# Optimization experiments

Measured on AMD Instinct MI355X. Metric: run time of the kernel, lower is better.

Reference implementation:

```python
import jax, jax.numpy as jnp
import numpy as np

N, E, DIN, DH = 50000, 1600000, 128, 128
P_DROP = 0.5


def setup_inputs() -> dict:
    key = jax.random.key(0)
    ks = jax.random.split(key, 9)
    scale = 0.05
    x = jax.random.normal(ks[0], (N, DIN), jnp.float32)
    edge_index = jax.random.randint(ks[1], (2, E), 0, N, dtype=jnp.int32)
    W0 = jax.random.normal(ks[2], (DH, DIN), jnp.float32) * scale
    b0 = jnp.zeros((DH,), jnp.float32)
    W1 = jax.random.normal(ks[3], (DH, DH), jnp.float32) * scale
    b1 = jnp.zeros((DH,), jnp.float32)
    W2 = jax.random.normal(ks[4], (DH, DH), jnp.float32) * scale
    b2 = jnp.zeros((DH,), jnp.float32)
    # deterministic inverted-dropout mask (train-mode Dropout(p=0.5))
    drop_mask = jax.random.bernoulli(ks[5], 1.0 - P_DROP, (N, DH)).astype(jnp.float32) / (1.0 - P_DROP)
    return {"x": x, "edge_index": edge_index, "drop_mask": drop_mask,
            "W0": W0, "b0": b0, "W1": W1, "b1": b1, "W2": W2, "b2": b2}


def _gcn_conv(h_in, W, b, src, dst, dinv):
    # PyG GCNConv: linear -> symmetric-normalized aggregation with self loops -> bias
    h = h_in @ W.T                                   # [N, out]
    norm = dinv[src] * dinv[dst]                      # [E]
    msg = h[src] * norm[:, None]                      # [E, out]
    out = jax.ops.segment_sum(msg, dst, num_segments=N)
    out = out + h * (dinv * dinv)[:, None]            # self-loop contribution
    return out + b


def reference(x, edge_index, drop_mask, W0, b0, W1, b1, W2, b2):
    src, dst = edge_index[0], edge_index[1]
    # degree of target nodes, +1 for the added self loop (shared by all layers)
    deg = jax.ops.segment_sum(jnp.ones((E,), x.dtype), dst, num_segments=N) + 1.0
    dinv = jax.lax.rsqrt(deg)

    h = _gcn_conv(x, W0, b0, src, dst, dinv)
    h = jax.nn.relu(h * drop_mask)                    # Dropout(0.5) then ReLU
    x_ = _gcn_conv(h, W1, b1, src, dst, dinv)
    x2 = _gcn_conv(h, W2, b2, src, dst, dinv)         # conv2 also consumes h (as in source)
    return (x_, x2)
```

## Files before the change

kernel.cpp:

```cpp
#include <hip/hip_runtime.h>


#define D 128
#define BK_SHIFT 7
#define BK_NODES 128
#define NBMAX 512
#define CAP 7936
#define TILE_A 2048

typedef __attribute__((ext_vector_type(8))) short bf16x8;
typedef __attribute__((ext_vector_type(4))) float f32x4;

static __device__ __forceinline__ unsigned f2bf(float f) {
  union { float f; unsigned u; } v; v.f = f;
  unsigned r = v.u + 0x7FFF + ((v.u >> 16) & 1);
  return r >> 16;
}
static __device__ __forceinline__ float bflo(unsigned u) {
  return __uint_as_float(u << 16);
}
static __device__ __forceinline__ float bfhi(unsigned u) {
  return __uint_as_float(u & 0xFFFF0000u);
}


__global__ __launch_bounds__(256) void k_bucketA(const int* __restrict__ src,
                                                 const int* __restrict__ dst,
                                                 int* __restrict__ bcnt,
                                                 int* __restrict__ packed,
                                                 const float* __restrict__ W0,
                                                 const float* __restrict__ W1,
                                                 const float* __restrict__ W2,
                                                 unsigned short* __restrict__ Wb,
                                                 int E, int nb) {
  __shared__ int hist[NBMAX];
  __shared__ int base[NBMAX];
  __shared__ unsigned pv[TILE_A];
  int t = threadIdx.x;
  int e0 = blockIdx.x * TILE_A;

  if (blockIdx.x < 192) {
    int i = blockIdx.x * 256 + t;
    const float* W = (i < 16384) ? W0 : (i < 32768 ? W1 : W2);
    Wb[i] = (unsigned short)f2bf(W[i & 16383]);
  }

  for (int b = t; b < nb; b += 256) hist[b] = 0;
  __syncthreads();

  for (int i = t; i < TILE_A; i += 256) {
    int e = e0 + i;
    if (e < E) {
      int d = dst[e];
      int s = src[e];
      unsigned bkt = (unsigned)d >> BK_SHIFT;
      pv[i] = (unsigned)(s & 0xFFFF) | ((unsigned)(d & (BK_NODES - 1)) << 16) |
              (bkt << 23);
      atomicAdd(&hist[bkt], 1);
    }
  }
  __syncthreads();

  for (int b = t; b < nb; b += 256) {
    int h = hist[b];
    if (h) base[b] = atomicAdd(&bcnt[b], h);
  }
  __syncthreads();

  for (int i = t; i < TILE_A; i += 256) {
    int e = e0 + i;
    if (e < E) {
      unsigned v = pv[i];
      unsigned bkt = v >> 23;
      int pos = atomicAdd(&base[bkt], 1);
      if (pos < CAP) packed[(size_t)bkt * CAP + pos] = (int)(v & 0x7FFFFF);
    }
  }
}

__global__ __launch_bounds__(512) void k_bucketB2(const int* __restrict__ packed,
                                                  const int* __restrict__ bcnt,
                                                  int* __restrict__ gcur,
                                                  int* __restrict__ srcSorted,
                                                  int* __restrict__ rowBeg,
                                                  int* __restrict__ rowEnd,
                                                  float* __restrict__ dinv,
                                                  int n) {
  __shared__ int histC[BK_NODES];
  __shared__ int cur[BK_NODES];
  __shared__ int buf[CAP];
  __shared__ int obase;
  int t = threadIdx.x;
  int bkt = blockIdx.x;
  int n0 = bkt << BK_SHIFT;
  int beg = bkt * CAP;
  int cnt = bcnt[bkt];
  if (cnt > CAP) cnt = CAP;

  if (t < BK_NODES) histC[t] = 0;
  __syncthreads();

  for (int i = t; i < cnt; i += 512)
    atomicAdd(&histC[packed[beg + i] >> 16], 1);
  __syncthreads();

  if (t == 0) {
    int run = 0;
#pragma unroll
    for (int j = 0; j < BK_NODES; ++j) { cur[j] = run; run += histC[j]; }
    obase = atomicAdd(gcur, run);
  }
  __syncthreads();

  if (t < BK_NODES && n0 + t < n) {
    int rb = obase + cur[t];
    rowBeg[n0 + t] = rb;
    rowEnd[n0 + t] = rb + histC[t];
    dinv[n0 + t]   = rsqrtf((float)histC[t] + 1.0f);
  }
  __syncthreads();

  for (int i = t; i < cnt; i += 512) {
    int p = packed[beg + i];
    int pos = atomicAdd(&cur[p >> 16], 1);
    buf[pos] = p & 0xFFFF;
  }
  __syncthreads();
  for (int i = t; i < cnt; i += 512)
    srcSorted[obase + i] = buf[i] << 8;
}


template <int EPI>
__global__ __launch_bounds__(256) void k_aggb(const unsigned* __restrict__ T,
                                              const int* __restrict__ srcSorted,
                                              const int* __restrict__ rowBeg,
                                              const int* __restrict__ rowEnd,
                                              const float* __restrict__ dinv,
                                              const float* __restrict__ bias,
                                              const float* __restrict__ mask,
                                              unsigned* __restrict__ outB,
                                              int n) {
  int wave = (blockIdx.x * 256 + threadIdx.x) >> 6;
  int lane = threadIdx.x & 63;
  if (wave >= n) return;
  const char* Tb = (const char*)T;
  int lo = lane << 2;
  int beg = rowBeg[wave], end = rowEnd[wave];
  float a0x = 0.f, a0y = 0.f, a1x = 0.f, a1y = 0.f;
  float a2x = 0.f, a2y = 0.f, a3x = 0.f, a3y = 0.f;
  int j = beg;
  for (; j + 15 < end; j += 16) {
    unsigned u[16];
#pragma unroll
    for (int q = 0; q < 16; ++q)
      u[q] = *(const unsigned*)(Tb + srcSorted[j + q] + lo);
#pragma unroll
    for (int q = 0; q < 16; q += 4) {
      a0x += bflo(u[q + 0]);  a0y += bfhi(u[q + 0]);
      a1x += bflo(u[q + 1]);  a1y += bfhi(u[q + 1]);
      a2x += bflo(u[q + 2]);  a2y += bfhi(u[q + 2]);
      a3x += bflo(u[q + 3]);  a3y += bfhi(u[q + 3]);
    }
  }
  for (; j + 7 < end; j += 8) {
    unsigned u[8];
#pragma unroll
    for (int q = 0; q < 8; ++q)
      u[q] = *(const unsigned*)(Tb + srcSorted[j + q] + lo);
#pragma unroll
    for (int q = 0; q < 8; q += 4) {
      a0x += bflo(u[q + 0]);  a0y += bfhi(u[q + 0]);
      a1x += bflo(u[q + 1]);  a1y += bfhi(u[q + 1]);
      a2x += bflo(u[q + 2]);  a2y += bfhi(u[q + 2]);
      a3x += bflo(u[q + 3]);  a3y += bfhi(u[q + 3]);
    }
  }
  for (; j < end; ++j) {
    unsigned u = *(const unsigned*)(Tb + srcSorted[j] + lo);
    a0x += bflo(u);
    a0y += bfhi(u);
  }
  unsigned us = T[(size_t)wave * 64 + lane];
  float dn = dinv[wave];
  float ox = ((a0x + a1x) + (a2x + a3x) + bflo(us)) * dn;
  float oy = ((a0y + a1y) + (a2y + a3y) + bfhi(us)) * dn;
  if (EPI == 1) {
    float2 bv = ((const float2*)bias)[lane];
    float2 mv = ((const float2*)mask)[(size_t)wave * 64 + lane];
    float hx = fmaxf((ox + bv.x) * mv.x, 0.f);
    float hy = fmaxf((oy + bv.y) * mv.y, 0.f);
    outB[(size_t)wave * 64 + lane] = f2bf(hx * dn) | (f2bf(hy * dn) << 16);
  } else {
    outB[(size_t)wave * 64 + lane] = f2bf(ox) | (f2bf(oy) << 16);
  }
}


template <bool BF16IN, bool BF16OUT>
__global__ __launch_bounds__(256) void k_gemm_mfma(const void* __restrict__ Xv,
                                                   const unsigned short* __restrict__ Wb,
                                                   const float* __restrict__ bias,
                                                   const float* __restrict__ prescale,
                                                   float* __restrict__ Cf,
                                                   unsigned short* __restrict__ Cb,
                                                   int nrows) {
  int wid  = threadIdx.x >> 6;
  int lane = threadIdx.x & 63;
  int r0   = blockIdx.x * 64 + wid * 16;
  int arow = r0 + (lane & 15);
  int kb   = (lane >> 4) * 8;
  bool rowok = arow < nrows;

  bf16x8 a[4];
  if (BF16IN) {
    const unsigned short* X = (const unsigned short*)Xv;
#pragma unroll
    for (int ks = 0; ks < 4; ++ks) {
      bf16x8 t;
      if (rowok) t = *reinterpret_cast<const bf16x8*>(X + (size_t)arow * D + ks * 32 + kb);
      else { for (int q = 0; q < 8; ++q) t[q] = 0; }
      a[ks] = t;
    }
  } else {
    const float* X = (const float*)Xv;
#pragma unroll
    for (int ks = 0; ks < 4; ++ks) {
      bf16x8 t;
      if (rowok) {
        const float* p = X + (size_t)arow * D + ks * 32 + kb;
        float4 f0 = *(const float4*)(p);
        float4 f1 = *(const float4*)(p + 4);
        t[0] = (short)f2bf(f0.x); t[1] = (short)f2bf(f0.y);
        t[2] = (short)f2bf(f0.z); t[3] = (short)f2bf(f0.w);
        t[4] = (short)f2bf(f1.x); t[5] = (short)f2bf(f1.y);
        t[6] = (short)f2bf(f1.z); t[7] = (short)f2bf(f1.w);
      } else {
        for (int q = 0; q < 8; ++q) t[q] = 0;
      }
      a[ks] = t;
    }
  }

  int rbase = r0 + (lane >> 4) * 4;
  float sc[4];
  if (BF16OUT) {
#pragma unroll
    for (int reg = 0; reg < 4; ++reg) {
      int rr = rbase + reg;
      sc[reg] = (prescale && rr < nrows) ? prescale[rr] : 1.0f;
    }
  }

#pragma unroll
  for (int ct = 0; ct < 8; ++ct) {
    int col = ct * 16 + (lane & 15);
    f32x4 acc = {0.f, 0.f, 0.f, 0.f};
#pragma unroll
    for (int ks = 0; ks < 4; ++ks) {
      bf16x8 b = *reinterpret_cast<const bf16x8*>(Wb + (size_t)col * D + ks * 32 + kb);
      acc = __builtin_amdgcn_mfma_f32_16x16x32_bf16(a[ks], b, acc, 0, 0, 0);
    }
    if (BF16OUT) {
#pragma unroll
      for (int reg = 0; reg < 4; ++reg) {
        int rr = rbase + reg;
        if (rr < nrows)
          Cb[(size_t)rr * D + col] = (unsigned short)f2bf(acc[reg] * sc[reg]);
      }
    } else {
      float bc = bias ? bias[col] : 0.f;
#pragma unroll
      for (int reg = 0; reg < 4; ++reg) {
        int rr = rbase + reg;
        if (rr < nrows) Cf[(size_t)rr * D + col] = acc[reg] + bc;
      }
    }
  }
}

__global__ __launch_bounds__(256) void k_gemm_mfma2(const unsigned short* __restrict__ X,
                                                    const unsigned short* __restrict__ W1b,
                                                    const unsigned short* __restrict__ W2b,
                                                    const float* __restrict__ b1,
                                                    const float* __restrict__ b2,
                                                    float* __restrict__ C1,
                                                    float* __restrict__ C2,
                                                    int nrows) {
  int wid  = threadIdx.x >> 6;
  int lane = threadIdx.x & 63;
  int r0   = blockIdx.x * 64 + wid * 16;
  int arow = r0 + (lane & 15);
  int kb   = (lane >> 4) * 8;
  bool rowok = arow < nrows;

  bf16x8 a[4];
#pragma unroll
  for (int ks = 0; ks < 4; ++ks) {
    bf16x8 t;
    if (rowok) t = *reinterpret_cast<const bf16x8*>(X + (size_t)arow * D + ks * 32 + kb);
    else { for (int q = 0; q < 8; ++q) t[q] = 0; }
    a[ks] = t;
  }

  int rbase = r0 + (lane >> 4) * 4;

#pragma unroll
  for (int wm = 0; wm < 2; ++wm) {
    const unsigned short* Wb = (wm == 0) ? W1b : W2b;
    const float* bias        = (wm == 0) ? b1 : b2;
    float* Cf                = (wm == 0) ? C1 : C2;
#pragma unroll
    for (int ct = 0; ct < 8; ++ct) {
      int col = ct * 16 + (lane & 15);
      f32x4 acc = {0.f, 0.f, 0.f, 0.f};
#pragma unroll
      for (int ks = 0; ks < 4; ++ks) {
        bf16x8 b = *reinterpret_cast<const bf16x8*>(Wb + (size_t)col * D + ks * 32 + kb);
        acc = __builtin_amdgcn_mfma_f32_16x16x32_bf16(a[ks], b, acc, 0, 0, 0);
      }
      float bc = bias[col];
#pragma unroll
      for (int reg = 0; reg < 4; ++reg) {
        int rr = rbase + reg;
        if (rr < nrows) Cf[(size_t)rr * D + col] = acc[reg] + bc;
      }
    }
  }
}


__global__ __launch_bounds__(256) void k_deg_f(const int* __restrict__ dst,
                                               float* __restrict__ deg, int E) {
  int i = blockIdx.x * 256 + threadIdx.x;
  if (i < E) atomicAdd(&deg[dst[i]], 1.0f);
}

__global__ __launch_bounds__(256) void k_dinv_f(float* __restrict__ deg, int n) {
  int i = blockIdx.x * 256 + threadIdx.x;
  if (i < n) deg[i] = rsqrtf(deg[i] + 1.0f);
}

__global__ __launch_bounds__(256) void k_selfmul(const float* __restrict__ X,
                                                 const float* __restrict__ dinv,
                                                 float* __restrict__ out, int n) {
  int i = blockIdx.x * 256 + threadIdx.x;
  if (i >= n * 32) return;
  int r = i >> 5, c4 = (i & 31) << 2;
  float di = dinv[r];
  float s = di * di;
  float4 h = *(const float4*)(X + (size_t)r * D + c4);
  h.x *= s; h.y *= s; h.z *= s; h.w *= s;
  *(float4*)(out + (size_t)r * D + c4) = h;
}

__global__ __launch_bounds__(256) void k_relumask(float* __restrict__ h,
                                                  const float* __restrict__ mask, int n) {
  int i = blockIdx.x * 256 + threadIdx.x;
  if (i >= n * 32) return;
  float4 v = *(const float4*)(h + (size_t)i * 4);
  float4 m = *(const float4*)(mask + (size_t)i * 4);
  v.x = fmaxf(v.x * m.x, 0.f);
  v.y = fmaxf(v.y * m.y, 0.f);
  v.z = fmaxf(v.z * m.z, 0.f);
  v.w = fmaxf(v.w * m.w, 0.f);
  *(float4*)(h + (size_t)i * 4) = v;
}

__global__ __launch_bounds__(256) void k_aggatomic(const float* __restrict__ X,
                                                   const int* __restrict__ src,
                                                   const int* __restrict__ dst,
                                                   const float* __restrict__ dinv,
                                                   float* __restrict__ out, int E) {
  int gid = blockIdx.x * 256 + threadIdx.x;
  int wave = gid >> 6;
  int lane = threadIdx.x & 63;
  int nw = (gridDim.x * 256) >> 6;
  for (int e = wave; e < E; e += nw) {
    int s = src[e], d = dst[e];
    float nrm = dinv[s] * dinv[d];
    float2 v = ((const float2*)(X + (size_t)s * D))[lane];
    float* op = out + (size_t)d * D + lane * 2;
    atomicAdd(op, v.x * nrm);
    atomicAdd(op + 1, v.y * nrm);
  }
}

__global__ __launch_bounds__(256) void k_addbias(float* __restrict__ C,
                                                 const float* __restrict__ bias, int n) {
  int i = blockIdx.x * 256 + threadIdx.x;
  if (i >= n * 32) return;
  int c4 = (i & 31) << 2;
  float4 v = *(const float4*)(C + (size_t)i * 4);
  float4 b = *(const float4*)(bias + c4);
  v.x += b.x; v.y += b.y; v.z += b.z; v.w += b.w;
  *(float4*)(C + (size_t)i * 4) = v;
}

template <bool BF16OUT>
__global__ __launch_bounds__(256) void k_gemm128(const float* __restrict__ X,
                                                 const float* __restrict__ W,
                                                 const float* __restrict__ bias,
                                                 const float* __restrict__ prescale,
                                                 float* __restrict__ Cf,
                                                 unsigned short* __restrict__ Cb,
                                                 int nrows) {
  __shared__ float Xs[64][132];
  __shared__ float Ws[32][128];

  int tid = threadIdx.x;
  int row0 = blockIdx.x * 64;

  for (int t = tid; t < 2048; t += 256) {
    int r = t >> 5;
    int c4 = (t & 31) << 2;
    int gr = row0 + r;
    float4 v = make_float4(0.f, 0.f, 0.f, 0.f);
    if (gr < nrows) v = *(const float4*)(X + (size_t)gr * D + c4);
    Xs[r][c4 + 0] = v.x; Xs[r][c4 + 1] = v.y;
    Xs[r][c4 + 2] = v.z; Xs[r][c4 + 3] = v.w;
  }

  float acc[4][8];
#pragma unroll
  for (int i = 0; i < 4; ++i)
#pragma unroll
    for (int j = 0; j < 8; ++j) acc[i][j] = 0.f;

  int ty = tid >> 4, tx = tid & 15;
  int r0 = ty << 2, c0 = tx << 3;

  for (int k0 = 0; k0 < 128; k0 += 32) {
    int j = tid >> 1;
    int kkb = (tid & 1) << 4;
    const float4* wp = (const float4*)(W + j * D + k0 + kkb);
    float4 wa = wp[0], wb = wp[1], wc = wp[2], wd = wp[3];

    __syncthreads();
    Ws[kkb +  0][j] = wa.x; Ws[kkb +  1][j] = wa.y; Ws[kkb +  2][j] = wa.z; Ws[kkb +  3][j] = wa.w;
    Ws[kkb +  4][j] = wb.x; Ws[kkb +  5][j] = wb.y; Ws[kkb +  6][j] = wb.z; Ws[kkb +  7][j] = wb.w;
    Ws[kkb +  8][j] = wc.x; Ws[kkb +  9][j] = wc.y; Ws[kkb + 10][j] = wc.z; Ws[kkb + 11][j] = wc.w;
    Ws[kkb + 12][j] = wd.x; Ws[kkb + 13][j] = wd.y; Ws[kkb + 14][j] = wd.z; Ws[kkb + 15][j] = wd.w;
    __syncthreads();

#pragma unroll
    for (int kk = 0; kk < 32; ++kk) {
      float xi[4];
      xi[0] = Xs[r0 + 0][k0 + kk];
      xi[1] = Xs[r0 + 1][k0 + kk];
      xi[2] = Xs[r0 + 2][k0 + kk];
      xi[3] = Xs[r0 + 3][k0 + kk];
      float4 wv0 = *(const float4*)(&Ws[kk][c0]);
      float4 wv1 = *(const float4*)(&Ws[kk][c0 + 4]);
      float wf[8] = {wv0.x, wv0.y, wv0.z, wv0.w, wv1.x, wv1.y, wv1.z, wv1.w};
#pragma unroll
      for (int i = 0; i < 4; ++i)
#pragma unroll
        for (int jj = 0; jj < 8; ++jj) acc[i][jj] += xi[i] * wf[jj];
    }
  }

  float4 bv0 = make_float4(0.f, 0.f, 0.f, 0.f);
  float4 bv1 = make_float4(0.f, 0.f, 0.f, 0.f);
  if (bias) {
    bv0 = *(const float4*)(bias + c0);
    bv1 = *(const float4*)(bias + c0 + 4);
  }

#pragma unroll
  for (int i = 0; i < 4; ++i) {
    int gr = row0 + r0 + i;
    if (gr < nrows) {
      float o[8];
      o[0] = acc[i][0] + bv0.x; o[1] = acc[i][1] + bv0.y;
      o[2] = acc[i][2] + bv0.z; o[3] = acc[i][3] + bv0.w;
      o[4] = acc[i][4] + bv1.x; o[5] = acc[i][5] + bv1.y;
      o[6] = acc[i][6] + bv1.z; o[7] = acc[i][7] + bv1.w;
      if (BF16OUT) {
        float dn = prescale ? prescale[gr] : 1.0f;
        uint4 pk;
        pk.x = f2bf(o[0] * dn) | (f2bf(o[1] * dn) << 16);
        pk.y = f2bf(o[2] * dn) | (f2bf(o[3] * dn) << 16);
        pk.z = f2bf(o[4] * dn) | (f2bf(o[5] * dn) << 16);
        pk.w = f2bf(o[6] * dn) | (f2bf(o[7] * dn) << 16);
        *(uint4*)(Cb + (size_t)gr * D + c0) = pk;
      } else {
        *(float4*)(Cf + (size_t)gr * D + c0)     = make_float4(o[0], o[1], o[2], o[3]);
        *(float4*)(Cf + (size_t)gr * D + c0 + 4) = make_float4(o[4], o[5], o[6], o[7]);
      }
    }
  }
}


extern "C" void kernel_launch(void* const* d_in, const int* in_sizes, int n_in,
                              void* d_out, int out_size, void* d_ws, size_t ws_size,
                              hipStream_t stream) {
  const float* x    = (const float*)d_in[0];
  const int*   ei   = (const int*)d_in[1];
  const float* mask = (const float*)d_in[2];
  const float* W0   = (const float*)d_in[3];
  const float* b0   = (const float*)d_in[4];
  const float* W1   = (const float*)d_in[5];
  const float* b1   = (const float*)d_in[6];
  const float* W2   = (const float*)d_in[7];
  const float* b2   = (const float*)d_in[8];

  const int N = in_sizes[0] / D;
  const int E = in_sizes[1] / 2;
  const int* srcv = ei;
  const int* dstv = ei + E;

  float* out  = (float*)d_out;
  float* outA = out;
  float* outB = out + (size_t)N * D;

  const size_t featBytes  = (size_t)N * D * sizeof(float);
  const size_t featBytesH = (size_t)N * D * sizeof(short);
  const int gGemm  = (N + 63) / 64;
  const int gEdge  = (E + 255) / 256;
  const int gNode  = (N + 255) / 256;
  const int gWaveN = (N + 3) / 4;
  const int gElem  = (N * 32 + 255) / 256;
  const int nb     = (N + BK_NODES - 1) >> BK_SHIFT;
  const int gBA    = (E + TILE_A - 1) / TILE_A;
  const size_t padBytes = (size_t)nb * CAP * 4;

  auto align256 = [](size_t v) { return (v + 255) & ~(size_t)255; };
  char* w = (char*)d_ws;
  size_t off = 0;
  int*   bcnt      = (int*)(w + off);   off = align256(off + (NBMAX + 1) * 4);
  int*   gcur      = bcnt + NBMAX;
  int*   rowBeg    = (int*)(w + off);   off = align256(off + (size_t)N * 4);
  int*   rowEnd    = (int*)(w + off);   off = align256(off + (size_t)N * 4);
  float* dinv      = (float*)(w + off); off = align256(off + (size_t)N * 4);
  int*   srcSorted = (int*)(w + off);   off = align256(off + (size_t)E * 4);
  unsigned short* Wb = (unsigned short*)(w + off); off = align256(off + 3 * 16384 * 2);
  unsigned* h0bf   = (unsigned*)(w + off); off = align256(off + featBytesH);
  unsigned* hbf    = (unsigned*)(w + off); off = align256(off + featBytesH);
  size_t gbfOff    = off;
  unsigned* gbf    = (unsigned*)(w + off);
  size_t offA = off + featBytesH;
  size_t offB = off + padBytes;
  off = align256(offA > offB ? offA : offB);
  int*   packed    = (int*)gbf;
  size_t need = off;
  (void)gbfOff;

  if (ws_size >= need && N <= 65536 && nb <= NBMAX &&
      (E / nb) + 1024 <= CAP) {
    hipMemsetAsync(bcnt, 0, (size_t)(NBMAX + 1) * sizeof(int), stream);
    k_bucketA<<<gBA, 256, 0, stream>>>(srcv, dstv, bcnt, packed,
                                       W0, W1, W2, Wb, E, nb);
    k_bucketB2<<<nb, 512, 0, stream>>>(packed, bcnt, gcur, srcSorted,
                                       rowBeg, rowEnd, dinv, N);

    k_gemm_mfma<false, true><<<gGemm, 256, 0, stream>>>(
        x, Wb, nullptr, dinv, nullptr, (unsigned short*)h0bf, N);
    k_aggb<1><<<gWaveN, 256, 0, stream>>>(h0bf, srcSorted, rowBeg, rowEnd,
                                          dinv, b0, mask, hbf, N);
    k_aggb<2><<<gWaveN, 256, 0, stream>>>(hbf, srcSorted, rowBeg, rowEnd,
                                          dinv, nullptr, nullptr, gbf, N);
    k_gemm_mfma2<<<gGemm, 256, 0, stream>>>(
        (const unsigned short*)gbf, Wb + 16384, Wb + 32768, b1, b2,
        outA, outB, N);
  } else {
    float* fdinv = (float*)(w);
    float* fA    = (float*)(w + 0x40000);
    float* fB    = (float*)((char*)fA + featBytes);
    hipMemsetAsync(fdinv, 0, (size_t)N * sizeof(float), stream);
    k_deg_f<<<gEdge, 256, 0, stream>>>(dstv, fdinv, E);
    k_dinv_f<<<gNode, 256, 0, stream>>>(fdinv, N);
    k_gemm128<false><<<gGemm, 256, 0, stream>>>(x, W0, nullptr, nullptr, fB, nullptr, N);
    k_selfmul<<<gElem, 256, 0, stream>>>(fB, fdinv, fA, N);
    k_aggatomic<<<4096, 256, 0, stream>>>(fB, srcv, dstv, fdinv, fA, E);
    k_addbias<<<gElem, 256, 0, stream>>>(fA, b0, N);
    k_relumask<<<gElem, 256, 0, stream>>>(fA, mask, N);
    k_selfmul<<<gElem, 256, 0, stream>>>(fA, fdinv, fB, N);
    k_aggatomic<<<4096, 256, 0, stream>>>(fA, srcv, dstv, fdinv, fB, E);
    k_gemm128<false><<<gGemm, 256, 0, stream>>>(fB, W1, b1, nullptr, outA, nullptr, N);
    k_gemm128<false><<<gGemm, 256, 0, stream>>>(fB, W2, b2, nullptr, outB, nullptr, N);
  }
}
```

Measured before the change: 223.5 us.

## Store bf16 features in column-chunked layout and split aggregation by chunk

Feature matrices are now stored as four column chunks of 32 bf16 values (64 bytes) per node, each chunk laid out contiguously across nodes. The GEMMs are changed to write and read this layout. Aggregation launches four times as many blocks, one per chunk. Within a wave, 16 lanes cover one 64-byte chunk row and the four lane groups take different edges, with a shuffle reduction at the end. The goal is a smaller gather footprint per pass, better cache locality, and more parallelism. The cost is four times the index reads and an extra reduction.

```diff
diff --git a/kernel.cpp b/kernel.cpp
--- a/kernel.cpp
+++ b/kernel.cpp
@@ -127,12 +127,12 @@
   }
   __syncthreads();
   for (int i = t; i < cnt; i += 512)
-    srcSorted[obase + i] = buf[i] << 8;
+    srcSorted[obase + i] = buf[i] << 6;
 }
 
 
 template <int EPI>
-__global__ __launch_bounds__(256) void k_aggb(const unsigned* __restrict__ T,
+__global__ __launch_bounds__(256) void k_aggc(const unsigned* __restrict__ T,
                                               const int* __restrict__ srcSorted,
                                               const int* __restrict__ rowBeg,
                                               const int* __restrict__ rowEnd,
@@ -140,71 +140,77 @@
                                               const float* __restrict__ bias,
                                               const float* __restrict__ mask,
                                               unsigned* __restrict__ outB,
-                                              int n) {
-  int wave = (blockIdx.x * 256 + threadIdx.x) >> 6;
+                                              int n, int nodeBlk) {
+  int c    = blockIdx.x / nodeBlk;
+  int nblk = blockIdx.x - c * nodeBlk;
+  int node = nblk * 4 + (threadIdx.x >> 6);
+  if (node >= n) return;
   int lane = threadIdx.x & 63;
-  if (wave >= n) return;
-  const char* Tb = (const char*)T;
-  int lo = lane << 2;
-  int beg = rowBeg[wave], end = rowEnd[wave];
-  float a0x = 0.f, a0y = 0.f, a1x = 0.f, a1y = 0.f;
-  float a2x = 0.f, a2y = 0.f, a3x = 0.f, a3y = 0.f;
+  int es   = lane >> 4;
+  int sl   = lane & 15;
+
+  const char* Tb = (const char*)T + (size_t)c * n * 64;
+  int slb = sl << 2;
+
+  int beg = rowBeg[node], end = rowEnd[node];
+  float ax = 0.f, ay = 0.f, bx = 0.f, by = 0.f;
   int j = beg;
   for (; j + 15 < end; j += 16) {
-    unsigned u[16];
-#pragma unroll
-    for (int q = 0; q < 16; ++q)
-      u[q] = *(const unsigned*)(Tb + srcSorted[j + q] + lo);
-#pragma unroll
-    for (int q = 0; q < 16; q += 4) {
-      a0x += bflo(u[q + 0]);  a0y += bfhi(u[q + 0]);
-      a1x += bflo(u[q + 1]);  a1y += bfhi(u[q + 1]);
-      a2x += bflo(u[q + 2]);  a2y += bfhi(u[q + 2]);
-      a3x += bflo(u[q + 3]);  a3y += bfhi(u[q + 3]);
-    }
-  }
-  for (; j + 7 < end; j += 8) {
-    unsigned u[8];
-#pragma unroll
-    for (int q = 0; q < 8; ++q)
-      u[q] = *(const unsigned*)(Tb + srcSorted[j + q] + lo);
-#pragma unroll
-    for (int q = 0; q < 8; q += 4) {
-      a0x += bflo(u[q + 0]);  a0y += bfhi(u[q + 0]);
-      a1x += bflo(u[q + 1]);  a1y += bfhi(u[q + 1]);
-      a2x += bflo(u[q + 2]);  a2y += bfhi(u[q + 2]);
-      a3x += bflo(u[q + 3]);  a3y += bfhi(u[q + 3]);
-    }
-  }
-  for (; j < end; ++j) {
-    unsigned u = *(const unsigned*)(Tb + srcSorted[j] + lo);
-    a0x += bflo(u);
-    a0y += bfhi(u);
-  }
-  unsigned us = T[(size_t)wave * 64 + lane];
-  float dn = dinv[wave];
-  float ox = ((a0x + a1x) + (a2x + a3x) + bflo(us)) * dn;
-  float oy = ((a0y + a1y) + (a2y + a3y) + bfhi(us)) * dn;
+    int o0 = srcSorted[j + es];
+    int o1 = srcSorted[j + 4 + es];
+    int o2 = srcSorted[j + 8 + es];
+    int o3 = srcSorted[j + 12 + es];
+    unsigned u0 = *(const unsigned*)(Tb + o0 + slb);
+    unsigned u1 = *(const unsigned*)(Tb + o1 + slb);
+    unsigned u2 = *(const unsigned*)(Tb + o2 + slb);
+    unsigned u3 = *(const unsigned*)(Tb + o3 + slb);
+    ax += bflo(u0) + bflo(u2);  ay += bfhi(u0) + bfhi(u2);
+    bx += bflo(u1) + bflo(u3);  by += bfhi(u1) + bfhi(u3);
+  }
+  for (; j + 3 < end; j += 4) {
+    int o = srcSorted[j + es];
+    unsigned u = *(const unsigned*)(Tb + o + slb);
+    ax += bflo(u);
+    ay += bfhi(u);
+  }
+  if (j + es < end) {
+    int o = srcSorted[j + es];
+    unsigned u = *(const unsigned*)(Tb + o + slb);
+    ax += bflo(u);
+    ay += bfhi(u);
+  }
+  if (es == 0) {
+    unsigned u = *(const unsigned*)(Tb + (node << 6) + slb);
+    ax += bflo(u);
+    ay += bfhi(u);
+  }
+  float sx = ax + bx, sy = ay + by;
+  sx += __shfl_xor(sx, 16);  sy += __shfl_xor(sy, 16);
+  sx += __shfl_xor(sx, 32);  sy += __shfl_xor(sy, 32);
+
+  float dn = dinv[node];
+  float ox = sx * dn;
+  float oy = sy * dn;
+  unsigned w;
   if (EPI == 1) {
-    float2 bv = ((const float2*)bias)[lane];
-    float2 mv = ((const float2*)mask)[(size_t)wave * 64 + lane];
+    float2 bv = ((const float2*)bias)[c * 16 + sl];
+    float2 mv = ((const float2*)mask)[(size_t)node * 64 + c * 16 + sl];
     float hx = fmaxf((ox + bv.x) * mv.x, 0.f);
     float hy = fmaxf((oy + bv.y) * mv.y, 0.f);
-    outB[(size_t)wave * 64 + lane] = f2bf(hx * dn) | (f2bf(hy * dn) << 16);
+    w = f2bf(hx * dn) | (f2bf(hy * dn) << 16);
   } else {
-    outB[(size_t)wave * 64 + lane] = f2bf(ox) | (f2bf(oy) << 16);
-  }
-}
-
-
-template <bool BF16IN, bool BF16OUT>
-__global__ __launch_bounds__(256) void k_gemm_mfma(const void* __restrict__ Xv,
-                                                   const unsigned short* __restrict__ Wb,
-                                                   const float* __restrict__ bias,
-                                                   const float* __restrict__ prescale,
-                                                   float* __restrict__ Cf,
-                                                   unsigned short* __restrict__ Cb,
-                                                   int nrows) {
+    w = f2bf(ox) | (f2bf(oy) << 16);
+  }
+  if (lane < 16)
+    outB[((size_t)c * n + node) * 16 + sl] = w;
+}
+
+
+__global__ __launch_bounds__(256) void k_gemm0(const float* __restrict__ X,
+                                               const unsigned short* __restrict__ Wb,
+                                               const float* __restrict__ prescale,
+                                               unsigned short* __restrict__ Cb,
+                                               int nrows) {
   int wid  = threadIdx.x >> 6;
   int lane = threadIdx.x & 63;
   int r0   = blockIdx.x * 64 + wid * 16;
@@ -213,43 +219,29 @@
   bool rowok = arow < nrows;
 
   bf16x8 a[4];
-  if (BF16IN) {
-    const unsigned short* X = (const unsigned short*)Xv;
-#pragma unroll
-    for (int ks = 0; ks < 4; ++ks) {
-      bf16x8 t;
-      if (rowok) t = *reinterpret_cast<const bf16x8*>(X + (size_t)arow * D + ks * 32 + kb);
-      else { for (int q = 0; q < 8; ++q) t[q] = 0; }
-      a[ks] = t;
-    }
-  } else {
-    const float* X = (const float*)Xv;
-#pragma unroll
-    for (int ks = 0; ks < 4; ++ks) {
-      bf16x8 t;
-      if (rowok) {
-        const float* p = X + (size_t)arow * D + ks * 32 + kb;
-        float4 f0 = *(const float4*)(p);
-        float4 f1 = *(const float4*)(p + 4);
-        t[0] = (short)f2bf(f0.x); t[1] = (short)f2bf(f0.y);
-        t[2] = (short)f2bf(f0.z); t[3] = (short)f2bf(f0.w);
-        t[4] = (short)f2bf(f1.x); t[5] = (short)f2bf(f1.y);
-        t[6] = (short)f2bf(f1.z); t[7] = (short)f2bf(f1.w);
-      } else {
-        for (int q = 0; q < 8; ++q) t[q] = 0;
-      }
-      a[ks] = t;
-    }
+#pragma unroll
+  for (int ks = 0; ks < 4; ++ks) {
+    bf16x8 t;
+    if (rowok) {
+      const float* p = X + (size_t)arow * D + ks * 32 + kb;
+      float4 f0 = *(const float4*)(p);
+      float4 f1 = *(const float4*)(p + 4);
+      t[0] = (short)f2bf(f0.x); t[1] = (short)f2bf(f0.y);
+      t[2] = (short)f2bf(f0.z); t[3] = (short)f2bf(f0.w);
+      t[4] = (short)f2bf(f1.x); t[5] = (short)f2bf(f1.y);
+      t[6] = (short)f2bf(f1.z); t[7] = (short)f2bf(f1.w);
+    } else {
+      for (int q = 0; q < 8; ++q) t[q] = 0;
+    }
+    a[ks] = t;
   }
 
   int rbase = r0 + (lane >> 4) * 4;
   float sc[4];
-  if (BF16OUT) {
-#pragma unroll
-    for (int reg = 0; reg < 4; ++reg) {
-      int rr = rbase + reg;
-      sc[reg] = (prescale && rr < nrows) ? prescale[rr] : 1.0f;
-    }
+#pragma unroll
+  for (int reg = 0; reg < 4; ++reg) {
+    int rr = rbase + reg;
+    sc[reg] = (rr < nrows) ? prescale[rr] : 1.0f;
   }
 
 #pragma unroll
@@ -261,20 +253,13 @@
       bf16x8 b = *reinterpret_cast<const bf16x8*>(Wb + (size_t)col * D + ks * 32 + kb);
       acc = __builtin_amdgcn_mfma_f32_16x16x32_bf16(a[ks], b, acc, 0, 0, 0);
     }
-    if (BF16OUT) {
-#pragma unroll
-      for (int reg = 0; reg < 4; ++reg) {
-        int rr = rbase + reg;
-        if (rr < nrows)
-          Cb[(size_t)rr * D + col] = (unsigned short)f2bf(acc[reg] * sc[reg]);
-      }
-    } else {
-      float bc = bias ? bias[col] : 0.f;
-#pragma unroll
-      for (int reg = 0; reg < 4; ++reg) {
-        int rr = rbase + reg;
-        if (rr < nrows) Cf[(size_t)rr * D + col] = acc[reg] + bc;
-      }
+    int cch = col >> 5, cin = col & 31;
+#pragma unroll
+    for (int reg = 0; reg < 4; ++reg) {
+      int rr = rbase + reg;
+      if (rr < nrows)
+        Cb[((size_t)cch * nrows + rr) * 32 + cin] =
+            (unsigned short)f2bf(acc[reg] * sc[reg]);
     }
   }
 }
@@ -298,7 +283,8 @@
 #pragma unroll
   for (int ks = 0; ks < 4; ++ks) {
     bf16x8 t;
-    if (rowok) t = *reinterpret_cast<const bf16x8*>(X + (size_t)arow * D + ks * 32 + kb);
+    if (rowok)
+      t = *reinterpret_cast<const bf16x8*>(X + ((size_t)ks * nrows + arow) * 32 + kb);
     else { for (int q = 0; q < 8; ++q) t[q] = 0; }
     a[ks] = t;
   }
@@ -397,13 +383,10 @@
   *(float4*)(C + (size_t)i * 4) = v;
 }
 
-template <bool BF16OUT>
 __global__ __launch_bounds__(256) void k_gemm128(const float* __restrict__ X,
                                                  const float* __restrict__ W,
                                                  const float* __restrict__ bias,
-                                                 const float* __restrict__ prescale,
                                                  float* __restrict__ Cf,
-                                                 unsigned short* __restrict__ Cb,
                                                  int nrows) {
   __shared__ float Xs[64][132];
   __shared__ float Ws[32][128];
@@ -471,23 +454,12 @@
   for (int i = 0; i < 4; ++i) {
     int gr = row0 + r0 + i;
     if (gr < nrows) {
-      float o[8];
-      o[0] = acc[i][0] + bv0.x; o[1] = acc[i][1] + bv0.y;
-      o[2] = acc[i][2] + bv0.z; o[3] = acc[i][3] + bv0.w;
-      o[4] = acc[i][4] + bv1.x; o[5] = acc[i][5] + bv1.y;
-      o[6] = acc[i][6] + bv1.z; o[7] = acc[i][7] + bv1.w;
-      if (BF16OUT) {
-        float dn = prescale ? prescale[gr] : 1.0f;
-        uint4 pk;
-        pk.x = f2bf(o[0] * dn) | (f2bf(o[1] * dn) << 16);
-        pk.y = f2bf(o[2] * dn) | (f2bf(o[3] * dn) << 16);
-        pk.z = f2bf(o[4] * dn) | (f2bf(o[5] * dn) << 16);
-        pk.w = f2bf(o[6] * dn) | (f2bf(o[7] * dn) << 16);
-        *(uint4*)(Cb + (size_t)gr * D + c0) = pk;
-      } else {
-        *(float4*)(Cf + (size_t)gr * D + c0)     = make_float4(o[0], o[1], o[2], o[3]);
-        *(float4*)(Cf + (size_t)gr * D + c0 + 4) = make_float4(o[4], o[5], o[6], o[7]);
-      }
+      *(float4*)(Cf + (size_t)gr * D + c0) =
+          make_float4(acc[i][0] + bv0.x, acc[i][1] + bv0.y,
+                      acc[i][2] + bv0.z, acc[i][3] + bv0.w);
+      *(float4*)(Cf + (size_t)gr * D + c0 + 4) =
+          make_float4(acc[i][4] + bv1.x, acc[i][5] + bv1.y,
+                      acc[i][6] + bv1.z, acc[i][7] + bv1.w);
     }
   }
 }
@@ -520,10 +492,11 @@
   const int gGemm  = (N + 63) / 64;
   const int gEdge  = (E + 255) / 256;
   const int gNode  = (N + 255) / 256;
-  const int gWaveN = (N + 3) / 4;
   const int gElem  = (N * 32 + 255) / 256;
   const int nb     = (N + BK_NODES - 1) >> BK_SHIFT;
   const int gBA    = (E + TILE_A - 1) / TILE_A;
+  const int nodeBlk = (N + 3) / 4;
+  const int gAgg   = nodeBlk * 4;
   const size_t padBytes = (size_t)nb * CAP * 4;
 
   auto align256 = [](size_t v) { return (v + 255) & ~(size_t)255; };
@@ -538,14 +511,12 @@
   unsigned short* Wb = (unsigned short*)(w + off); off = align256(off + 3 * 16384 * 2);
   unsigned* h0bf   = (unsigned*)(w + off); off = align256(off + featBytesH);
   unsigned* hbf    = (unsigned*)(w + off); off = align256(off + featBytesH);
-  size_t gbfOff    = off;
   unsigned* gbf    = (unsigned*)(w + off);
   size_t offA = off + featBytesH;
   size_t offB = off + padBytes;
   off = align256(offA > offB ? offA : offB);
   int*   packed    = (int*)gbf;
   size_t need = off;
-  (void)gbfOff;
 
   if (ws_size >= need && N <= 65536 && nb <= NBMAX &&
       (E / nb) + 1024 <= CAP) {
@@ -555,12 +526,11 @@
     k_bucketB2<<<nb, 512, 0, stream>>>(packed, bcnt, gcur, srcSorted,
                                        rowBeg, rowEnd, dinv, N);
 
-    k_gemm_mfma<false, true><<<gGemm, 256, 0, stream>>>(
-        x, Wb, nullptr, dinv, nullptr, (unsigned short*)h0bf, N);
-    k_aggb<1><<<gWaveN, 256, 0, stream>>>(h0bf, srcSorted, rowBeg, rowEnd,
-                                          dinv, b0, mask, hbf, N);
-    k_aggb<2><<<gWaveN, 256, 0, stream>>>(hbf, srcSorted, rowBeg, rowEnd,
-                                          dinv, nullptr, nullptr, gbf, N);
+    k_gemm0<<<gGemm, 256, 0, stream>>>(x, Wb, dinv, (unsigned short*)h0bf, N);
+    k_aggc<1><<<gAgg, 256, 0, stream>>>(h0bf, srcSorted, rowBeg, rowEnd,
+                                        dinv, b0, mask, hbf, N, nodeBlk);
+    k_aggc<2><<<gAgg, 256, 0, stream>>>(hbf, srcSorted, rowBeg, rowEnd,
+                                        dinv, nullptr, nullptr, gbf, N, nodeBlk);
     k_gemm_mfma2<<<gGemm, 256, 0, stream>>>(
         (const unsigned short*)gbf, Wb + 16384, Wb + 32768, b1, b2,
         outA, outB, N);
@@ -571,14 +541,14 @@
     hipMemsetAsync(fdinv, 0, (size_t)N * sizeof(float), stream);
     k_deg_f<<<gEdge, 256, 0, stream>>>(dstv, fdinv, E);
     k_dinv_f<<<gNode, 256, 0, stream>>>(fdinv, N);
-    k_gemm128<false><<<gGemm, 256, 0, stream>>>(x, W0, nullptr, nullptr, fB, nullptr, N);
+    k_gemm128<<<gGemm, 256, 0, stream>>>(x, W0, nullptr, fB, N);
     k_selfmul<<<gElem, 256, 0, stream>>>(fB, fdinv, fA, N);
     k_aggatomic<<<4096, 256, 0, stream>>>(fB, srcv, dstv, fdinv, fA, E);
     k_addbias<<<gElem, 256, 0, stream>>>(fA, b0, N);
     k_relumask<<<gElem, 256, 0, stream>>>(fA, mask, N);
     k_selfmul<<<gElem, 256, 0, stream>>>(fA, fdinv, fB, N);
     k_aggatomic<<<4096, 256, 0, stream>>>(fA, srcv, dstv, fdinv, fB, E);
-    k_gemm128<false><<<gGemm, 256, 0, stream>>>(fB, W1, b1, nullptr, outA, nullptr, N);
-    k_gemm128<false><<<gGemm, 256, 0, stream>>>(fB, W2, b2, nullptr, outB, nullptr, N);
-  }
-}
+    k_gemm128<<<gGemm, 256, 0, stream>>>(fB, W1, b1, outA, N);
+    k_gemm128<<<gGemm, 256, 0, stream>>>(fB, W2, b2, outB, N);
+  }
+}
```

Measured after the change: 314.7 us. +40.8%, slower.
